# Kernel tuning notes

Hardware: AMD Instinct MI355X
Metric: run time of the kernel (lower is better)

## Reference

```python
import jax, jax.numpy as jnp
import numpy as np


def setup_inputs() -> dict:
    key = jax.random.key(0)
    k1, k2 = jax.random.split(key)
    B, D, H, W = 4, 64, 64, 64
    M = 4096
    z = jax.random.normal(k1, (B, D, H, W), dtype=jnp.float32)
    e = jax.random.normal(k2, (M, D), dtype=jnp.float32)
    log_sigma = jnp.zeros((1,), dtype=jnp.float32)
    return {"z": z, "e": e, "log_sigma": log_sigma}


def reference(z, e, log_sigma):
    # z: [B, D, H, W] latents, e: [M, D] codebook, log_sigma: [1] parameter
    T = 1.0  # latent_temp default
    B, D, H, W = z.shape
    zf = jnp.transpose(z, (0, 2, 3, 1)).reshape(-1, D)  # [N, D]
    N = zf.shape[0]
    # squared pairwise distances via ||z||^2 + ||e||^2 - 2 z e^T (avoids [N,M,D] intermediate)
    d2 = (jnp.sum(zf * zf, axis=1)[:, None]
          + jnp.sum(e * e, axis=1)[None, :]
          - 2.0 * zf @ e.T)  # [N, M]
    alpha = -1.0 / (2.0 * jnp.exp(log_sigma[0]) ** 2)
    matrix = alpha * d2 / T  # [N, M]
    lse = jax.nn.logsumexp(matrix, axis=0)  # [M], reduce over N points per code
    # np.log(np.e) == 1.0
    loss = (-jnp.mean(T * lse)
            + 0.5 * D * (2.0 * log_sigma[0] - 1.0)
            + jnp.log(jnp.asarray(N, dtype=jnp.float32)))
    return loss
```

## Files before the change

### kernel.cpp

```cpp
#include <hip/hip_runtime.h>
#include <hip/hip_bf16.h>
#include <math.h>

#define D_   64
#define HW_  4096
#define N_   16384
#define M_   4096

#define AEN_OFF 0
#define SUM_OFF 4096
#define EBF_OFF 8192
#define WS_FLOATS (EBF_OFF + 131072)

#define L2E 1.4426950408889634f

typedef __attribute__((ext_vector_type(8))) short short8;
typedef __attribute__((ext_vector_type(16))) float floatx16;

#if __has_builtin(__builtin_amdgcn_exp2f)
#define EXP2F(x) __builtin_amdgcn_exp2f(x)
#else
#define EXP2F(x) exp2f(x)
#endif

__device__ __forceinline__ unsigned int bf16_rne(float x) {
    unsigned int u = __float_as_uint(x);
    u += 0x7fffu + ((u >> 16) & 1u);
    return u >> 16;
}

__global__ void prep_e(const float* __restrict__ e,
                       const float* __restrict__ lsp,
                       float* __restrict__ ws) {
    const float ls = lsp[0];
    const float alpha = -0.5f * __expf(-2.f * ls);
    const float anl = alpha * L2E;
    unsigned short* ebf = (unsigned short*)(ws + EBF_OFF);
    int m = blockIdx.x * 256 + threadIdx.x;
    const float4* ep = (const float4*)(e + (size_t)m * D_);
    float s = 0.f;
    unsigned int pk[32];
#pragma unroll
    for (int k = 0; k < 16; ++k) {
        float4 v = ep[k];
        s += v.x * v.x + v.y * v.y + v.z * v.z + v.w * v.w;
        pk[2 * k]     = bf16_rne(v.x) | (bf16_rne(v.y) << 16);
        pk[2 * k + 1] = bf16_rne(v.z) | (bf16_rne(v.w) << 16);
    }
    uint4* op = (uint4*)(ebf + (size_t)m * 64);
#pragma unroll
    for (int k = 0; k < 8; ++k)
        op[k] = make_uint4(pk[4 * k], pk[4 * k + 1], pk[4 * k + 2], pk[4 * k + 3]);
    ws[AEN_OFF + m] = anl * s;
    ws[SUM_OFF + m] = 0.f;
}

__global__ __launch_bounds__(256, 3) void main_fast(
        const float* __restrict__ z, const float* __restrict__ lsp,
        float* __restrict__ ws) {
    __shared__ unsigned short zlds[32 * 64];
    __shared__ float azn_lds[32];

    const unsigned short* ebf = (const unsigned short*)(ws + EBF_OFF);
    const float* aen = ws + AEN_OFF;
    float* sums = ws + SUM_OFF;

    const int t = threadIdx.x;
    const int lane = t & 63;
    const int w = t >> 6;
    const int rlo = lane & 31;
    const int kh = lane >> 5;
    const int bx = (int)blockIdx.x;

    const float ls = lsp[0];
    const float alpha = -0.5f * __expf(-2.f * ls);
    const float anl = alpha * L2E;
    const float c2p = -2.f * alpha * L2E;

    const int n0 = bx * 32;
    const int b = n0 >> 12, hw0 = n0 & 4095;

    {
        const int g = t & 7;
        const int db = t >> 3;
        float part[4] = {0.f, 0.f, 0.f, 0.f};
#pragma unroll
        for (int h = 0; h < 2; ++h) {
            int d = db + 32 * h;
            float4 v = *(const float4*)(z + ((size_t)(b * D_ + d)) * HW_ + hw0 + g * 4);
            float vv[4] = {v.x, v.y, v.z, v.w};
#pragma unroll
            for (int q = 0; q < 4; ++q) {
                int hw = g * 4 + q;
                int unit = hw * 8 + ((d >> 3) ^ (hw & 7));
                zlds[unit * 8 + (d & 7)] = (unsigned short)bf16_rne(vv[q] * c2p);
                part[q] = fmaf(vv[q], vv[q], part[q]);
            }
        }
#pragma unroll
        for (int q = 0; q < 4; ++q) {
            part[q] += __shfl_xor(part[q], 8);
            part[q] += __shfl_xor(part[q], 16);
            part[q] += __shfl_xor(part[q], 32);
        }
        if (t < 32) azn_lds[t] = 0.f;
        __syncthreads();
        if (lane < 8) {
#pragma unroll
            for (int q = 0; q < 4; ++q)
                atomicAdd(&azn_lds[lane * 4 + q], part[q]);
        }
        __syncthreads();
    }

    short8 af[4];
#pragma unroll
    for (int ks = 0; ks < 4; ++ks) {
        int unit = rlo * 8 + ((ks * 2 + kh) ^ (rlo & 7));
        af[ks] = *(const short8*)&zlds[unit * 8];
    }
    float azn_r[16];
#pragma unroll
    for (int rg = 0; rg < 4; ++rg) {
        float4 vv = *(const float4*)&azn_lds[4 * kh + 8 * rg];
        azn_r[rg * 4 + 0] = vv.x * anl; azn_r[rg * 4 + 1] = vv.y * anl;
        azn_r[rg * 4 + 2] = vv.z * anl; azn_r[rg * 4 + 3] = vv.w * anl;
    }

    short8 bfc[2][4]; float aenc[2];
    {
        int mt = w + 4 * (bx & 15);
        int m0 = mt * 64;
#pragma unroll
        for (int ms = 0; ms < 2; ++ms) {
            int row = m0 + ms * 32 + rlo;
            aenc[ms] = aen[row];
#pragma unroll
            for (int ks = 0; ks < 4; ++ks)
                bfc[ms][ks] = *(const short8*)(ebf + (size_t)row * 64 + (ks * 2 + kh) * 8);
        }
    }

    for (int j = 0; j < 16; ++j) {
        short8 bfn[2][4]; float aenn[2];
        if (j < 15) {
            int mt = w + 4 * ((j + 1 + bx) & 15);
            int m0 = mt * 64;
#pragma unroll
            for (int ms = 0; ms < 2; ++ms) {
                int row = m0 + ms * 32 + rlo;
                aenn[ms] = aen[row];
#pragma unroll
                for (int ks = 0; ks < 4; ++ks)
                    bfn[ms][ks] = *(const short8*)(ebf + (size_t)row * 64 + (ks * 2 + kh) * 8);
            }
        }

        floatx16 acc[2];
#pragma unroll
        for (int ms = 0; ms < 2; ++ms)
#pragma unroll
            for (int r = 0; r < 16; ++r)
                acc[ms][r] = azn_r[r] + aenc[ms];

#pragma unroll
        for (int ks = 0; ks < 4; ++ks)
#pragma unroll
            for (int ms = 0; ms < 2; ++ms)
                acc[ms] = __builtin_amdgcn_mfma_f32_32x32x16_bf16(
                    af[ks], bfc[ms][ks], acc[ms], 0, 0, 0);

        float s0 = 0.f, s1 = 0.f;
#pragma unroll
        for (int r = 0; r < 16; ++r) s0 += EXP2F(acc[0][r]);
#pragma unroll
        for (int r = 0; r < 16; ++r) s1 += EXP2F(acc[1][r]);
        s0 += __shfl_down(s0, 32);
        s1 += __shfl_down(s1, 32);

        int mt = w + 4 * ((j + bx) & 15);
        int m0 = mt * 64;
        if (lane < 32) {
            atomicAdd(&sums[m0 + lane], s0);
            atomicAdd(&sums[m0 + 32 + lane], s1);
        }

#pragma unroll
        for (int ms = 0; ms < 2; ++ms) {
            aenc[ms] = aenn[ms];
#pragma unroll
            for (int ks = 0; ks < 4; ++ks) bfc[ms][ks] = bfn[ms][ks];
        }
    }
}

__global__ void finalize_fast(const float* __restrict__ ws,
                              const float* __restrict__ lsp,
                              float* __restrict__ out) {
    __shared__ double red[256];
    const float* sums = ws + SUM_OFF;
    int t = threadIdx.x;
    double local = 0.0;
#pragma unroll
    for (int j = 0; j < 16; ++j) {
        float s = sums[t + 256 * j];
        local += (double)logf(s);
    }
    red[t] = local;
    __syncthreads();
    for (int off = 128; off > 0; off >>= 1) {
        if (t < off) red[t] += red[t + off];
        __syncthreads();
    }
    if (t == 0) {
        double ls = (double)lsp[0];
        double loss = -(red[0] / (double)M_)
                      + 0.5 * (double)D_ * (2.0 * ls - 1.0)
                      + log((double)N_);
        out[0] = (float)loss;
    }
}

extern "C" void kernel_launch(void* const* d_in, const int* in_sizes, int n_in,
                              void* d_out, int out_size, void* d_ws, size_t ws_size,
                              hipStream_t stream) {
    const float* z   = (const float*)d_in[0];
    const float* e   = (const float*)d_in[1];
    const float* lsp = (const float*)d_in[2];
    float* ws  = (float*)d_ws;
    float* out = (float*)d_out;

    hipLaunchKernelGGL(prep_e, dim3(16), dim3(256), 0, stream, e, lsp, ws);
    hipLaunchKernelGGL(main_fast, dim3(N_ / 32), dim3(256), 0, stream, z, lsp, ws);
    hipLaunchKernelGGL(finalize_fast, dim3(1), dim3(256), 0, stream, ws, lsp, out);
}
```

Measured before the change: 95.41 us.

## Precompute bf16 z tiles and make codebook stationary with N-split grid

The prep kernel now also transposes z through LDS into a bf16 [N,64] buffer with scaled row norms. The main kernel keeps a 128-code tile of the codebook in registers and streams 1024 points per block across a 32x16 grid. It accumulates exp sums locally and reduces once per block through LDS before one global atomic per code. This replaces a per-tile global atomic, removes the per-block z transpose and the codebook reloads. It also moves the constant ||e||^2 term out of the inner loop into the finalize log. The cost is an extra 2 MB workspace round trip for z and lower occupancy (launch bounds 2).

Result: faster. 82.46 us (-13.6%).

```diff
diff --git a/kernel.cpp b/kernel.cpp
--- a/kernel.cpp
+++ b/kernel.cpp
@@ -7,12 +7,20 @@
 #define N_   16384
 #define M_   4096
 
-#define AEN_OFF 0
-#define SUM_OFF 4096
-#define EBF_OFF 8192
+#define BM 128
+#define NSPLIT 16
+#define NCHUNK (N_ / NSPLIT)
+#define NTILES (NCHUNK / 128)
+
+#define AZN_OFF 0
+#define AEN_OFF 16384
+#define SUM_OFF 20480
+#define ZTB_OFF 24576
+#define EBF_OFF (24576 + 524288)
 #define WS_FLOATS (EBF_OFF + 131072)
 
 #define L2E 1.4426950408889634f
+#define LN2 0.6931471805599453
 
 typedef __attribute__((ext_vector_type(8))) short short8;
 typedef __attribute__((ext_vector_type(16))) float floatx16;
@@ -29,169 +37,172 @@
     return u >> 16;
 }
 
-__global__ void prep_e(const float* __restrict__ e,
-                       const float* __restrict__ lsp,
-                       float* __restrict__ ws) {
+__global__ void prep_kernel(const float* __restrict__ z,
+                            const float* __restrict__ e,
+                            const float* __restrict__ lsp,
+                            float* __restrict__ ws) {
     const float ls = lsp[0];
     const float alpha = -0.5f * __expf(-2.f * ls);
     const float anl = alpha * L2E;
+    const float c2p = -2.f * alpha * L2E;
+    unsigned short* zTb = (unsigned short*)(ws + ZTB_OFF);
     unsigned short* ebf = (unsigned short*)(ws + EBF_OFF);
-    int m = blockIdx.x * 256 + threadIdx.x;
-    const float4* ep = (const float4*)(e + (size_t)m * D_);
-    float s = 0.f;
-    unsigned int pk[32];
-#pragma unroll
-    for (int k = 0; k < 16; ++k) {
-        float4 v = ep[k];
-        s += v.x * v.x + v.y * v.y + v.z * v.z + v.w * v.w;
-        pk[2 * k]     = bf16_rne(v.x) | (bf16_rne(v.y) << 16);
-        pk[2 * k + 1] = bf16_rne(v.z) | (bf16_rne(v.w) << 16);
-    }
-    uint4* op = (uint4*)(ebf + (size_t)m * 64);
-#pragma unroll
-    for (int k = 0; k < 8; ++k)
-        op[k] = make_uint4(pk[4 * k], pk[4 * k + 1], pk[4 * k + 2], pk[4 * k + 3]);
-    ws[AEN_OFF + m] = anl * s;
-    ws[SUM_OFF + m] = 0.f;
-}
-
-__global__ __launch_bounds__(256, 3) void main_fast(
-        const float* __restrict__ z, const float* __restrict__ lsp,
-        float* __restrict__ ws) {
-    __shared__ unsigned short zlds[32 * 64];
-    __shared__ float azn_lds[32];
-
+    const int blk = blockIdx.x, t = threadIdx.x;
+
+    if (blk < 256) {
+        __shared__ float lt[64 * 65];
+        const int b = blk >> 6, hw0 = (blk & 63) * 64;
+        const int n0 = b * HW_ + hw0;
+        const float* zb = z + ((size_t)b * D_) * HW_ + hw0;
+#pragma unroll
+        for (int i = 0; i < 4; ++i) {
+            int idx = t + 256 * i;
+            int d = idx >> 4, c = (idx & 15) * 4;
+            float4 v = *(const float4*)(zb + (size_t)d * HW_ + c);
+            float* p = &lt[d * 65 + c];
+            p[0] = v.x; p[1] = v.y; p[2] = v.z; p[3] = v.w;
+        }
+        __syncthreads();
+#pragma unroll
+        for (int j = 0; j < 2; ++j) {
+            int idx = t + 256 * j;
+            int nl = idx >> 3, g = idx & 7;
+            float v[8]; float s = 0.f;
+#pragma unroll
+            for (int jj = 0; jj < 8; ++jj) {
+                v[jj] = lt[(8 * g + jj) * 65 + nl];
+                s = fmaf(v[jj], v[jj], s);
+            }
+            s += __shfl_xor(s, 1);
+            s += __shfl_xor(s, 2);
+            s += __shfl_xor(s, 4);
+            uint4 pk;
+            pk.x = bf16_rne(v[0] * c2p) | (bf16_rne(v[1] * c2p) << 16);
+            pk.y = bf16_rne(v[2] * c2p) | (bf16_rne(v[3] * c2p) << 16);
+            pk.z = bf16_rne(v[4] * c2p) | (bf16_rne(v[5] * c2p) << 16);
+            pk.w = bf16_rne(v[6] * c2p) | (bf16_rne(v[7] * c2p) << 16);
+            *(uint4*)(zTb + (size_t)(n0 + nl) * 64 + 8 * g) = pk;
+            if (g == 0) ws[AZN_OFF + n0 + nl] = anl * s;
+        }
+    } else {
+        int m = (blk - 256) * 256 + t;
+        const float4* ep = (const float4*)(e + (size_t)m * D_);
+        float s = 0.f;
+        unsigned int pk[32];
+#pragma unroll
+        for (int k = 0; k < 16; ++k) {
+            float4 v = ep[k];
+            s += v.x * v.x + v.y * v.y + v.z * v.z + v.w * v.w;
+            pk[2 * k]     = bf16_rne(v.x) | (bf16_rne(v.y) << 16);
+            pk[2 * k + 1] = bf16_rne(v.z) | (bf16_rne(v.w) << 16);
+        }
+        uint4* op = (uint4*)(ebf + (size_t)m * 64);
+#pragma unroll
+        for (int k = 0; k < 8; ++k)
+            op[k] = make_uint4(pk[4 * k], pk[4 * k + 1], pk[4 * k + 2], pk[4 * k + 3]);
+        ws[AEN_OFF + m] = anl * s;
+        ws[SUM_OFF + m] = 0.f;
+    }
+}
+
+__global__ __launch_bounds__(256, 2) void main_fast(float* __restrict__ ws) {
+    __shared__ float lds_red[BM];
+    const unsigned short* zTb = (const unsigned short*)(ws + ZTB_OFF);
     const unsigned short* ebf = (const unsigned short*)(ws + EBF_OFF);
-    const float* aen = ws + AEN_OFF;
+    const float* azn = ws + AZN_OFF;
     float* sums = ws + SUM_OFF;
 
+    const int m0 = blockIdx.x * BM;
+    const int ns = blockIdx.y;
     const int t = threadIdx.x;
     const int lane = t & 63;
     const int w = t >> 6;
     const int rlo = lane & 31;
     const int kh = lane >> 5;
-    const int bx = (int)blockIdx.x;
-
-    const float ls = lsp[0];
-    const float alpha = -0.5f * __expf(-2.f * ls);
-    const float anl = alpha * L2E;
-    const float c2p = -2.f * alpha * L2E;
-
-    const int n0 = bx * 32;
-    const int b = n0 >> 12, hw0 = n0 & 4095;
-
+
+    short8 bf[4][4];
+#pragma unroll
+    for (int mt = 0; mt < 4; ++mt) {
+        int row = m0 + mt * 32 + rlo;
+#pragma unroll
+        for (int ks = 0; ks < 4; ++ks)
+            bf[mt][ks] = *(const short8*)(ebf + (size_t)row * 64 + (ks * 2 + kh) * 8);
+    }
+
+    float sum[4] = {0.f, 0.f, 0.f, 0.f};
+    const int nbase = ns * NCHUNK + w * 32;
+
+    short8 afc[4];
+    float4 aznc[4];
     {
-        const int g = t & 7;
-        const int db = t >> 3;
-        float part[4] = {0.f, 0.f, 0.f, 0.f};
-#pragma unroll
-        for (int h = 0; h < 2; ++h) {
-            int d = db + 32 * h;
-            float4 v = *(const float4*)(z + ((size_t)(b * D_ + d)) * HW_ + hw0 + g * 4);
-            float vv[4] = {v.x, v.y, v.z, v.w};
-#pragma unroll
-            for (int q = 0; q < 4; ++q) {
-                int hw = g * 4 + q;
-                int unit = hw * 8 + ((d >> 3) ^ (hw & 7));
-                zlds[unit * 8 + (d & 7)] = (unsigned short)bf16_rne(vv[q] * c2p);
-                part[q] = fmaf(vv[q], vv[q], part[q]);
-            }
-        }
-#pragma unroll
-        for (int q = 0; q < 4; ++q) {
-            part[q] += __shfl_xor(part[q], 8);
-            part[q] += __shfl_xor(part[q], 16);
-            part[q] += __shfl_xor(part[q], 32);
-        }
-        if (t < 32) azn_lds[t] = 0.f;
-        __syncthreads();
-        if (lane < 8) {
-#pragma unroll
-            for (int q = 0; q < 4; ++q)
-                atomicAdd(&azn_lds[lane * 4 + q], part[q]);
-        }
-        __syncthreads();
-    }
-
-    short8 af[4];
-#pragma unroll
-    for (int ks = 0; ks < 4; ++ks) {
-        int unit = rlo * 8 + ((ks * 2 + kh) ^ (rlo & 7));
-        af[ks] = *(const short8*)&zlds[unit * 8];
-    }
-    float azn_r[16];
-#pragma unroll
-    for (int rg = 0; rg < 4; ++rg) {
-        float4 vv = *(const float4*)&azn_lds[4 * kh + 8 * rg];
-        azn_r[rg * 4 + 0] = vv.x * anl; azn_r[rg * 4 + 1] = vv.y * anl;
-        azn_r[rg * 4 + 2] = vv.z * anl; azn_r[rg * 4 + 3] = vv.w * anl;
-    }
-
-    short8 bfc[2][4]; float aenc[2];
-    {
-        int mt = w + 4 * (bx & 15);
-        int m0 = mt * 64;
-#pragma unroll
-        for (int ms = 0; ms < 2; ++ms) {
-            int row = m0 + ms * 32 + rlo;
-            aenc[ms] = aen[row];
+#pragma unroll
+        for (int ks = 0; ks < 4; ++ks)
+            afc[ks] = *(const short8*)(zTb + (size_t)(nbase + rlo) * 64 + (ks * 2 + kh) * 8);
+        const int r0 = nbase + 4 * kh;
+#pragma unroll
+        for (int rg = 0; rg < 4; ++rg) aznc[rg] = *(const float4*)(azn + r0 + 8 * rg);
+    }
+
+#pragma unroll
+    for (int tile = 0; tile < NTILES; ++tile) {
+        short8 afn[4];
+        float4 aznn[4];
+        if (tile + 1 < NTILES) {
+            const int nr = nbase + (tile + 1) * 128;
 #pragma unroll
             for (int ks = 0; ks < 4; ++ks)
-                bfc[ms][ks] = *(const short8*)(ebf + (size_t)row * 64 + (ks * 2 + kh) * 8);
-        }
-    }
-
-    for (int j = 0; j < 16; ++j) {
-        short8 bfn[2][4]; float aenn[2];
-        if (j < 15) {
-            int mt = w + 4 * ((j + 1 + bx) & 15);
-            int m0 = mt * 64;
-#pragma unroll
-            for (int ms = 0; ms < 2; ++ms) {
-                int row = m0 + ms * 32 + rlo;
-                aenn[ms] = aen[row];
-#pragma unroll
-                for (int ks = 0; ks < 4; ++ks)
-                    bfn[ms][ks] = *(const short8*)(ebf + (size_t)row * 64 + (ks * 2 + kh) * 8);
-            }
-        }
-
-        floatx16 acc[2];
-#pragma unroll
-        for (int ms = 0; ms < 2; ++ms)
+                afn[ks] = *(const short8*)(zTb + (size_t)(nr + rlo) * 64 + (ks * 2 + kh) * 8);
+            const int r0 = nr + 4 * kh;
+#pragma unroll
+            for (int rg = 0; rg < 4; ++rg) aznn[rg] = *(const float4*)(azn + r0 + 8 * rg);
+        }
+
+        float azn_r[16];
+#pragma unroll
+        for (int rg = 0; rg < 4; ++rg) {
+            azn_r[rg * 4 + 0] = aznc[rg].x; azn_r[rg * 4 + 1] = aznc[rg].y;
+            azn_r[rg * 4 + 2] = aznc[rg].z; azn_r[rg * 4 + 3] = aznc[rg].w;
+        }
+
+        floatx16 acc[4];
+#pragma unroll
+        for (int mt = 0; mt < 4; ++mt)
 #pragma unroll
             for (int r = 0; r < 16; ++r)
-                acc[ms][r] = azn_r[r] + aenc[ms];
+                acc[mt][r] = azn_r[r];
 
 #pragma unroll
         for (int ks = 0; ks < 4; ++ks)
 #pragma unroll
-            for (int ms = 0; ms < 2; ++ms)
-                acc[ms] = __builtin_amdgcn_mfma_f32_32x32x16_bf16(
-                    af[ks], bfc[ms][ks], acc[ms], 0, 0, 0);
-
-        float s0 = 0.f, s1 = 0.f;
-#pragma unroll
-        for (int r = 0; r < 16; ++r) s0 += EXP2F(acc[0][r]);
-#pragma unroll
-        for (int r = 0; r < 16; ++r) s1 += EXP2F(acc[1][r]);
-        s0 += __shfl_down(s0, 32);
-        s1 += __shfl_down(s1, 32);
-
-        int mt = w + 4 * ((j + bx) & 15);
-        int m0 = mt * 64;
-        if (lane < 32) {
-            atomicAdd(&sums[m0 + lane], s0);
-            atomicAdd(&sums[m0 + 32 + lane], s1);
-        }
-
-#pragma unroll
-        for (int ms = 0; ms < 2; ++ms) {
-            aenc[ms] = aenn[ms];
-#pragma unroll
-            for (int ks = 0; ks < 4; ++ks) bfc[ms][ks] = bfn[ms][ks];
-        }
-    }
+            for (int mt = 0; mt < 4; ++mt)
+                acc[mt] = __builtin_amdgcn_mfma_f32_32x32x16_bf16(
+                    afc[ks], bf[mt][ks], acc[mt], 0, 0, 0);
+
+#pragma unroll
+        for (int mt = 0; mt < 4; ++mt) {
+            float s = 0.f;
+#pragma unroll
+            for (int r = 0; r < 16; ++r) s += EXP2F(acc[mt][r]);
+            sum[mt] += s;
+        }
+
+#pragma unroll
+        for (int ks = 0; ks < 4; ++ks) afc[ks] = afn[ks];
+#pragma unroll
+        for (int rg = 0; rg < 4; ++rg) aznc[rg] = aznn[rg];
+    }
+
+#pragma unroll
+    for (int mt = 0; mt < 4; ++mt) sum[mt] += __shfl_down(sum[mt], 32);
+
+    if (t < BM) lds_red[t] = 0.f;
+    __syncthreads();
+    if (lane < 32) {
+#pragma unroll
+        for (int mt = 0; mt < 4; ++mt) atomicAdd(&lds_red[mt * 32 + rlo], sum[mt]);
+    }
+    __syncthreads();
+    if (t < BM) atomicAdd(&sums[m0 + t], lds_red[t]);
 }
 
 __global__ void finalize_fast(const float* __restrict__ ws,
@@ -199,12 +210,13 @@
                               float* __restrict__ out) {
     __shared__ double red[256];
     const float* sums = ws + SUM_OFF;
+    const float* aen = ws + AEN_OFF;
     int t = threadIdx.x;
     double local = 0.0;
 #pragma unroll
     for (int j = 0; j < 16; ++j) {
-        float s = sums[t + 256 * j];
-        local += (double)logf(s);
+        int m = t + 256 * j;
+        local += (double)(aen[m] + log2f(sums[m]));
     }
     red[t] = local;
     __syncthreads();
@@ -214,7 +226,7 @@
     }
     if (t == 0) {
         double ls = (double)lsp[0];
-        double loss = -(red[0] / (double)M_)
+        double loss = -(LN2 * red[0] / (double)M_)
                       + 0.5 * (double)D_ * (2.0 * ls - 1.0)
                       + log((double)N_);
         out[0] = (float)loss;
@@ -230,7 +242,7 @@
     float* ws  = (float*)d_ws;
     float* out = (float*)d_out;
 
-    hipLaunchKernelGGL(prep_e, dim3(16), dim3(256), 0, stream, e, lsp, ws);
-    hipLaunchKernelGGL(main_fast, dim3(N_ / 32), dim3(256), 0, stream, z, lsp, ws);
+    hipLaunchKernelGGL(prep_kernel, dim3(272), dim3(256), 0, stream, z, e, lsp, ws);
+    hipLaunchKernelGGL(main_fast, dim3(M_ / BM, NSPLIT), dim3(256), 0, stream, ws);
     hipLaunchKernelGGL(finalize_fast, dim3(1), dim3(256), 0, stream, ws, lsp, out);
 }
```
